# Kernel tuning notes

Measured on AMD Instinct MI355X. Metric: run time of the kernel, lower is better.

## Reference

```python
import jax, jax.numpy as jnp
import numpy as np

IGST = 10      # ghost-cell width (module-level constant in the source)
EPS = 0.01     # tol passed to NeuralODE -> runge_kutta eps
W_SCALE = 0.05 # keep the learned stencil contractive over 100 steps


def cal_boundry(u):
    # Replace the IGST ghost cells on each side with the nearest interior value.
    m, n, l = u.shape
    left = jnp.broadcast_to(u[:, :, IGST:IGST + 1], (m, n, IGST))
    right = jnp.broadcast_to(u[:, :, -IGST - 1:-IGST], (m, n, IGST))
    return jnp.concatenate([left, u[:, :, IGST:-IGST], right], axis=2)


def stencil_f(z, W):
    # func: learned 1D stencil = same-padded conv over the spatial axis.
    # z: [m, n, l], W: [n_out, n_in, k]
    return jax.lax.conv_general_dilated(
        z, W, window_strides=(1,), padding='SAME',
        dimension_numbers=('NCH', 'OIH', 'NCH'))


def setup_inputs() -> dict:
    key = jax.random.key(0)
    k1, k2 = jax.random.split(key)
    z0 = jax.random.normal(k1, (32, 16, 8192), dtype=jnp.float32)
    W = jax.random.normal(k2, (16, 16, 5), dtype=jnp.float32) * W_SCALE
    return {'z0': z0, 'W': W, 't1_t0': 1}


def reference(z0, W, t1_t0):
    # SSP-RK3 (Shu-Osher) explicit time stepping with ghost-cell BCs.
    n_steps = int(round(t1_t0 / EPS))
    h = t1_t0 / n_steps

    def step(z, _):
        k1 = cal_boundry(z + h * stencil_f(z, W))
        k2 = cal_boundry(0.75 * z + 0.25 * k1 + 0.25 * h * stencil_f(k1, W))
        z_new = cal_boundry(z / 3.0 + 2.0 * k2 / 3.0 + 2.0 * h * stencil_f(k2, W) / 3.0)
        return z_new, None

    z, _ = jax.lax.scan(step, z0, None, length=n_steps)
    return z
```

## Files before the change

kernel.cpp:

```cpp
#include <hip/hip_runtime.h>


#define NCH    16
#define LL     8192
#define TX     128
#define HALOC  32
#define SLABC  192
#define NBX    64
#define NB     32
#define NSTEPS 100
#define SPK    5
#define NKER   (NSTEPS / SPK)

#define RAD    30
#define NCHUNK 31
#define ISLAB  190

typedef __bf16 bf16x8 __attribute__((ext_vector_type(8)));
typedef __bf16 bf16x4 __attribute__((ext_vector_type(4)));
typedef float  f32x4  __attribute__((ext_vector_type(4)));

__device__ __align__(16) float g_G [ 5*256];
__device__ __align__(16) float g_G2[ 9*256];
__device__ __align__(16) float g_Tp[13*256];
__device__ __align__(16) float g_T2[25*256];
__device__ __align__(16) float g_T3[37*256];
__device__ __align__(16) float g_T4[49*256];
__device__ __align__(16) float g_T5[61*256];
__device__ __align__(16) __bf16 g_Sfrag[NCHUNK*64*8];

__global__ void build_G(const float* __restrict__ W, const int* __restrict__ tptr) {
  const float h = (float)(*tptr) / (float)NSTEPS;
  const int o = threadIdx.x >> 4, i = threadIdx.x & 15;
#pragma unroll
  for (int k = 0; k < 5; ++k)
    g_G[k*256 + o*16 + i] = h * W[o*80 + i*5 + k];
}

__global__ void compose_k(int mode) {
  const float* A; int ra; const float* B; int rb; float* C;
  switch (mode) {
    case 0:  A = g_G;  ra = 2;  B = g_G;  rb = 2; C = g_G2; break;
    case 1:  A = g_G2; ra = 4;  B = g_G;  rb = 2; C = g_Tp; break;
    case 2:  A = g_Tp; ra = 6;  B = g_Tp; rb = 6; C = g_T2; break;
    case 3:  A = g_T2; ra = 12; B = g_Tp; rb = 6; C = g_T3; break;
    case 4:  A = g_T3; ra = 18; B = g_Tp; rb = 6; C = g_T4; break;
    default: A = g_T4; ra = 24; B = g_Tp; rb = 6; C = g_T5; break;
  }
  const int rc = ra + rb;
  const int d = (int)blockIdx.x - rc;
  const int o = threadIdx.x >> 4, i = threadIdx.x & 15;
  float acc = 0.f;
  for (int a = -ra; a <= ra; ++a) {
    const int b = d - a;
    if (b < -rb || b > rb) continue;
    const float* Am = A + (a+ra)*256 + o*16;
    const float* Bm = B + (b+rb)*256 + i;
#pragma unroll
    for (int j = 0; j < 16; ++j) acc += Am[j] * Bm[j*16];
  }
  C[(size_t)blockIdx.x*256 + o*16 + i] = acc;
}

__global__ void build_Tp() {
  const int o = threadIdx.x >> 4, i = threadIdx.x & 15;
#pragma unroll
  for (int k = 0; k < 13; ++k) {
    const int d = k - 6;
    float v = g_Tp[k*256 + o*16 + i] * (1.f/6.f);
    if (d >= -4 && d <= 4) v += 0.5f * g_G2[(d+4)*256 + o*16 + i];
    if (d >= -2 && d <= 2) v += g_G[(d+2)*256 + o*16 + i];
    g_Tp[k*256 + o*16 + i] = v;
  }
}

__device__ __forceinline__ float padread(const float* M, int r, int d, int oi) {
  return (d >= -r && d <= r) ? M[(d+r)*256 + oi] : 0.f;
}

__global__ void pack_S() {
  const int c = blockIdx.x;
  const int lane = threadIdx.x & 63;
  const int jj = (threadIdx.x >> 6) * 2;
  const int gg = lane >> 4, n = lane & 15;
  const int k = 2*c + (gg >> 1);
  const int d = k - RAD;
#pragma unroll
  for (int u = 0; u < 2; ++u) {
    const int j = jj + u;
    const int i = (gg & 1)*8 + j;
    const int oi = n*16 + i;
    float v = 0.f;
    if (k <= 60) {
      v = 5.f  * padread(g_Tp,  6, d, oi)
        + 10.f * padread(g_T2, 12, d, oi)
        + 10.f * padread(g_T3, 18, d, oi)
        + 5.f  * padread(g_T4, 24, d, oi)
        +        padread(g_T5, 30, d, oi);
    }
    g_Sfrag[((size_t)c*64 + lane)*8 + j] = (__bf16)v;
  }
}

__device__ __forceinline__ int ldsIdx(int col, int ch) {
  return col * NCH + (ch ^ ((col & 4) << 1));
}

__global__ __launch_bounds__(256) void transpose_kernel(const float* __restrict__ in,
                                                        float* __restrict__ out) {
  const int b = blockIdx.y;
  const int x = blockIdx.x * 256 + threadIdx.x;
  const float* __restrict__ ib = in + (size_t)b * NCH * LL;
  float* __restrict__ ob = out + (size_t)b * NCH * LL;
  float v[NCH];
#pragma unroll
  for (int c = 0; c < NCH; ++c) v[c] = ib[c * LL + x];
#pragma unroll
  for (int c = 0; c < NCH; c += 4)
    *(float4*)(ob + (size_t)x * NCH + c) = make_float4(v[c], v[c+1], v[c+2], v[c+3]);
}

__device__ __forceinline__ bf16x8 mkA(const float* __restrict__ W, int c, int g, int n) {
  const int kk = c * 2 + (g >> 1);
  bf16x8 a;
#pragma unroll
  for (int j = 0; j < 8; ++j) {
    const int i = (g & 1) * 8 + j;
    a[j] = (__bf16)((kk < 5) ? W[n * (NCH * 5) + i * 5 + kk] : 0.0f);
  }
  return a;
}

__device__ __forceinline__ f32x4 ldState(const float* __restrict__ zb, int x0,
                                         int t, int n, int g) {
  int gx = x0 - HALOC + 16 * t + n;
  gx = min(max(gx, 0), LL - 1);
  return *(const f32x4*)(zb + (size_t)gx * NCH + g * 4);
}

template<int MODE, bool UPDZ>
__device__ __forceinline__ void tileStage(
    int t, f32x4& KZ, f32x4& KF, float az, float ak, float agh,
    const __bf16* __restrict__ RS, __bf16* __restrict__ WS,
    bf16x8 af0, bf16x8 af1, bf16x8 af2,
    int lane, int g, int n, bool leftE, bool rightE,
    float* __restrict__ ob, int x0, int finalKer)
{
  f32x4 acc = {0.f, 0.f, 0.f, 0.f};
#pragma unroll
  for (int c = 0; c < 3; ++c) {
    const int kk = c * 2 + (g >> 1);
    int s = 16 * t + n + kk - 2;
    s = min(max(s, 0), SLABC - 1);
    const bf16x8 bfrag = *(const bf16x8*)(&RS[ldsIdx(s, (g & 1) * 8)]);
    const bf16x8 a = (c == 0) ? af0 : (c == 1) ? af1 : af2;
    acc = __builtin_amdgcn_mfma_f32_16x16x32_bf16(a, bfrag, acc, 0, 0, 0);
  }
  f32x4 v;
#pragma unroll
  for (int r = 0; r < 4; ++r) v[r] = az * KZ[r] + ak * KF[r] + agh * acc[r];

  if (leftE && t == 2) {
#pragma unroll
    for (int r = 0; r < 4; ++r) {
      const float sv = __shfl(v[r], (lane & 48) | 10, 64);
      if (n < 10) v[r] = sv;
    }
  }
  if (rightE && t == 9) {
#pragma unroll
    for (int r = 0; r < 4; ++r) {
      const float sv = __shfl(v[r], (lane & 48) | 5, 64);
      if (n > 5) v[r] = sv;
    }
  }

  KF = v;
  if (UPDZ) KZ = v;

  if (MODE == 0) {
    bf16x4 bv = { (__bf16)v[0], (__bf16)v[1], (__bf16)v[2], (__bf16)v[3] };
    *(bf16x4*)(&WS[ldsIdx(16 * t + n, g * 4)]) = bv;
  } else {
    if (t >= 2 && t <= 9) {
      const int xg = x0 - HALOC + 16 * t + n;
      if (!finalKer) {
        *(f32x4*)(ob + (size_t)xg * NCH + g * 4) = v;
      } else {
#pragma unroll
        for (int r = 0; r < 4; ++r) ob[(size_t)(g * 4 + r) * LL + xg] = v[r];
      }
    }
  }
}

#define STAGE(az, ak, agh, UPDZ, MODE)                                          \
  do {                                                                          \
    const __bf16* RS_ = S[rb];                                                  \
    __bf16* WS_ = S[rb ^ 1];                                                    \
    tileStage<MODE, UPDZ>(wv + 0, kz0, kf0, az, ak, agh, RS_, WS_, af0, af1,    \
                          af2, lane, g, n, leftE, rightE, ob, x0, finalKer);    \
    tileStage<MODE, UPDZ>(wv + 4, kz1, kf1, az, ak, agh, RS_, WS_, af0, af1,    \
                          af2, lane, g, n, leftE, rightE, ob, x0, finalKer);    \
    tileStage<MODE, UPDZ>(wv + 8, kz2, kf2, az, ak, agh, RS_, WS_, af0, af1,    \
                          af2, lane, g, n, leftE, rightE, ob, x0, finalKer);    \
  } while (0)

__global__ __launch_bounds__(256)
void multistep_kernel(
    const float* __restrict__ zin,
    float* __restrict__ zout,
    const float* __restrict__ W,
    const int* __restrict__ tptr, int finalKer)
{
  __shared__ __align__(16) __bf16 S[2][SLABC * NCH];
  __shared__ __align__(16) __bf16 ISL[ISLAB * NCH];

  const int b = blockIdx.y, bx = blockIdx.x;
  const int x0 = bx * TX;
  const bool leftE = (bx == 0), rightE = (bx == NBX - 1);
  const int tid = threadIdx.x, lane = tid & 63, wv = tid >> 6;
  const int g = lane >> 4, n = lane & 15;

  const float* __restrict__ zb = zin + (size_t)b * NCH * LL;
  float* __restrict__ ob = zout + (size_t)b * NCH * LL;

  if (leftE || rightE) {
    const float h = (float)(*tptr) / (float)NSTEPS;
    const bf16x8 af0 = mkA(W, 0, g, n);
    const bf16x8 af1 = mkA(W, 1, g, n);
    const bf16x8 af2 = mkA(W, 2, g, n);

    for (int q = tid; q < SLABC * 4; q += 256) {
      const int s = q >> 2, cg = (q & 3) * 4;
      int gx = x0 - HALOC + s;
      gx = min(max(gx, 0), LL - 1);
      const float4 v = *(const float4*)(zb + (size_t)gx * NCH + cg);
      bf16x4 bv = { (__bf16)v.x, (__bf16)v.y, (__bf16)v.z, (__bf16)v.w };
      *(bf16x4*)(&S[0][ldsIdx(s, cg)]) = bv;
    }

    f32x4 kz0 = ldState(zb, x0, wv + 0, n, g);
    f32x4 kz1 = ldState(zb, x0, wv + 4, n, g);
    f32x4 kz2 = ldState(zb, x0, wv + 8, n, g);
    f32x4 kf0 = {0.f,0.f,0.f,0.f}, kf1 = kf0, kf2 = kf0;
    __syncthreads();

    const float c13 = 1.0f / 3.0f, c23 = 2.0f / 3.0f;
    int rb = 0;
#pragma unroll 1
    for (int sp = 0; sp < SPK; ++sp) {
      STAGE(1.0f, 0.0f, h, false, 0);
      __syncthreads(); rb ^= 1;
      STAGE(0.75f, 0.25f, 0.25f * h, false, 0);
      __syncthreads(); rb ^= 1;
      if (sp != SPK - 1) {
        STAGE(c13, c23, c23 * h, true, 0);
        __syncthreads(); rb ^= 1;
      } else {
        STAGE(c13, c23, c23 * h, true, 1);
      }
    }
  } else {
    for (int q = tid; q < ISLAB * 4; q += 256) {
      const int s = q >> 2, cg = (q & 3) * 4;
      const int gx = x0 - RAD + s;
      const float4 v = *(const float4*)(zb + (size_t)gx * NCH + cg);
      bf16x4 bv = { (__bf16)v.x, (__bf16)v.y, (__bf16)v.z, (__bf16)v.w };
      *(bf16x4*)(&ISL[ldsIdx(s, cg)]) = bv;
    }

    const int o0 = 16 * wv + n;
    const f32x4 kz0 = *(const f32x4*)(zb + (size_t)(x0 + o0) * NCH + g * 4);
    const f32x4 kz1 = *(const f32x4*)(zb + (size_t)(x0 + o0 + 64) * NCH + g * 4);
    __syncthreads();

    const int p = g >> 1, hsel = g & 1;
    f32x4 acc0 = {0.f,0.f,0.f,0.f}, acc1 = acc0;
    const __bf16* Af = g_Sfrag + (size_t)lane * 8;
    int col0 = o0 + p;
#pragma unroll
    for (int c = 0; c < NCHUNK; ++c) {
      const bf16x8 a = *(const bf16x8*)(Af + (size_t)c * 512);
      const int xr = ((((col0 >> 2) & 1) ^ hsel) << 4);
      const bf16x8 b0 = *(const bf16x8*)((const char*)ISL + col0 * 32 + xr);
      const bf16x8 b1 = *(const bf16x8*)((const char*)ISL + (col0 + 64) * 32 + xr);
      acc0 = __builtin_amdgcn_mfma_f32_16x16x32_bf16(a, b0, acc0, 0, 0, 0);
      acc1 = __builtin_amdgcn_mfma_f32_16x16x32_bf16(a, b1, acc1, 0, 0, 0);
      col0 += 2;
    }

    f32x4 v0, v1;
#pragma unroll
    for (int r = 0; r < 4; ++r) { v0[r] = kz0[r] + acc0[r]; v1[r] = kz1[r] + acc1[r]; }

    if (!finalKer) {
      *(f32x4*)(ob + (size_t)(x0 + o0) * NCH + g * 4) = v0;
      *(f32x4*)(ob + (size_t)(x0 + o0 + 64) * NCH + g * 4) = v1;
    } else {
#pragma unroll
      for (int r = 0; r < 4; ++r) {
        ob[(size_t)(g * 4 + r) * LL + (x0 + o0)] = v0[r];
        ob[(size_t)(g * 4 + r) * LL + (x0 + o0 + 64)] = v1[r];
      }
    }
  }
}

extern "C" void kernel_launch(void* const* d_in, const int* in_sizes, int n_in,
                              void* d_out, int out_size, void* d_ws, size_t ws_size,
                              hipStream_t stream) {
  const float* z0 = (const float*)d_in[0];
  const float* W  = (const float*)d_in[1];
  const int*   t  = (const int*)d_in[2];

  float* Q = (float*)d_out;
  float* P = (float*)d_ws;

  build_G<<<dim3(1), dim3(256), 0, stream>>>(W, t);
  compose_k<<<dim3( 9), dim3(256), 0, stream>>>(0);
  compose_k<<<dim3(13), dim3(256), 0, stream>>>(1);
  build_Tp<<<dim3(1), dim3(256), 0, stream>>>();
  compose_k<<<dim3(25), dim3(256), 0, stream>>>(2);
  compose_k<<<dim3(37), dim3(256), 0, stream>>>(3);
  compose_k<<<dim3(49), dim3(256), 0, stream>>>(4);
  compose_k<<<dim3(61), dim3(256), 0, stream>>>(5);
  pack_S<<<dim3(NCHUNK), dim3(256), 0, stream>>>();

  dim3 block(256);
  transpose_kernel<<<dim3(32, NB), block, 0, stream>>>(z0, Q);

  dim3 mgrid(NBX, NB);
  for (int k = 1; k <= NKER; ++k) {
    if (k & 1) multistep_kernel<<<mgrid, block, 0, stream>>>(Q, P, W, t, 0);
    else       multistep_kernel<<<mgrid, block, 0, stream>>>(P, Q, W, t, k == NKER);
  }
}
```

Before: 801.2 us.

## Precompute boundary-block propagators and replace iterative edge blocks with dense matvec

```diff
diff --git a/kernel.cpp b/kernel.cpp
--- a/kernel.cpp
+++ b/kernel.cpp
@@ -4,8 +4,6 @@
 #define NCH    16
 #define LL     8192
 #define TX     128
-#define HALOC  32
-#define SLABC  192
 #define NBX    64
 #define NB     32
 #define NSTEPS 100
@@ -15,6 +13,11 @@
 #define RAD    30
 #define NCHUNK 31
 #define ISLAB  190
+
+#define WCOLS  96
+#define DWIN   1072
+#define NROWS  592
+#define EBLK   4
 
 typedef __bf16 bf16x8 __attribute__((ext_vector_type(8)));
 typedef __bf16 bf16x4 __attribute__((ext_vector_type(4)));
@@ -28,6 +31,8 @@
 __device__ __align__(16) float g_T4[49*256];
 __device__ __align__(16) float g_T5[61*256];
 __device__ __align__(16) __bf16 g_Sfrag[NCHUNK*64*8];
+__device__ __align__(16) float g_CL[(size_t)NROWS*DWIN];
+__device__ __align__(16) float g_CR[(size_t)NROWS*DWIN];
 
 __global__ void build_G(const float* __restrict__ W, const int* __restrict__ tptr) {
   const float h = (float)(*tptr) / (float)NSTEPS;
@@ -106,6 +111,108 @@
   return col * NCH + (ch ^ ((col & 4) << 1));
 }
 
+__device__ __forceinline__ bf16x8 mkA(const float* __restrict__ W, int c, int g, int n) {
+  const int kk = c * 2 + (g >> 1);
+  bf16x8 a;
+#pragma unroll
+  for (int j = 0; j < 8; ++j) {
+    const int i = (g & 1) * 8 + j;
+    a[j] = (__bf16)((kk < 5) ? W[n * (NCH * 5) + i * 5 + kk] : 0.0f);
+  }
+  return a;
+}
+
+__global__ __launch_bounds__(384)
+void edge_evolve(const float* __restrict__ W, const int* __restrict__ tptr) {
+  __shared__ __align__(16) __bf16 ES[2][WCOLS * NCH];
+  const int j = blockIdx.x, e = blockIdx.y;
+  const float h = (float)(*tptr) / (float)NSTEPS;
+  const int tid = threadIdx.x, lane = tid & 63, wv = tid >> 6;
+  const int g = lane >> 4, n = lane & 15;
+  const int t = wv, mycol = 16 * t + n;
+  const int cwj = (e ? 29 : 0) + (j >> 4), chj = j & 15;
+
+  const bf16x8 af0 = mkA(W, 0, g, n);
+  const bf16x8 af1 = mkA(W, 1, g, n);
+  const bf16x8 af2 = mkA(W, 2, g, n);
+
+  const int hot = ldsIdx(cwj, chj);
+  for (int q = tid; q < WCOLS * NCH; q += 384)
+    ES[0][q] = (__bf16)(q == hot ? 1.f : 0.f);
+
+  f32x4 kz = {0.f, 0.f, 0.f, 0.f};
+  if (mycol == cwj && g == (chj >> 2)) kz[chj & 3] = 1.f;
+  f32x4 kf = {0.f, 0.f, 0.f, 0.f};
+  __syncthreads();
+
+  const float c13 = 1.0f / 3.0f, c23 = 2.0f / 3.0f;
+  int rb = 0;
+#pragma unroll 1
+  for (int sp = 0; sp < SPK; ++sp) {
+#pragma unroll 1
+    for (int st = 0; st < 3; ++st) {
+      const float az  = (st == 0) ? 1.0f : (st == 1) ? 0.75f : c13;
+      const float ak  = (st == 0) ? 0.0f : (st == 1) ? 0.25f : c23;
+      const float agh = (st == 0) ? h    : (st == 1) ? 0.25f*h : c23*h;
+      const __bf16* RS = ES[rb];
+      __bf16* WS = ES[rb ^ 1];
+      f32x4 acc = {0.f, 0.f, 0.f, 0.f};
+#pragma unroll
+      for (int c = 0; c < 3; ++c) {
+        const int kk = c * 2 + (g >> 1);
+        int s = mycol + kk - 2;
+        s = min(max(s, 0), WCOLS - 1);
+        const bf16x8 bfrag = *(const bf16x8*)(&RS[ldsIdx(s, (g & 1) * 8)]);
+        const bf16x8 a = (c == 0) ? af0 : (c == 1) ? af1 : af2;
+        acc = __builtin_amdgcn_mfma_f32_16x16x32_bf16(a, bfrag, acc, 0, 0, 0);
+      }
+      f32x4 v;
+#pragma unroll
+      for (int r = 0; r < 4; ++r) v[r] = az * kz[r] + ak * kf[r] + agh * acc[r];
+      if (e == 0 && t == 0) {
+#pragma unroll
+        for (int r = 0; r < 4; ++r) {
+          const float sv = __shfl(v[r], (lane & 48) | 10, 64);
+          if (n < 10) v[r] = sv;
+        }
+      }
+      if (e == 1 && t == 5) {
+#pragma unroll
+        for (int r = 0; r < 4; ++r) {
+          const float sv = __shfl(v[r], (lane & 48) | 5, 64);
+          if (n > 5) v[r] = sv;
+        }
+      }
+      kf = v;
+      if (st == 2) kz = v;
+      bf16x4 bv = { (__bf16)v[0], (__bf16)v[1], (__bf16)v[2], (__bf16)v[3] };
+      *(bf16x4*)(&WS[ldsIdx(mycol, g * 4)]) = bv;
+      __syncthreads();
+      rb ^= 1;
+    }
+  }
+
+  if (e == 0) {
+    if (mycol <= 36) {
+      const int rowb = mycol * 16 + g * 4;
+#pragma unroll
+      for (int r = 0; r < 4; ++r) {
+        const float id = (mycol == cwj && (g * 4 + r) == chj) ? 1.f : 0.f;
+        g_CL[(size_t)(rowb + r) * DWIN + j] = kz[r] - id;
+      }
+    }
+  } else {
+    if (mycol >= 59) {
+      const int rowb = (mycol - 59) * 16 + g * 4;
+#pragma unroll
+      for (int r = 0; r < 4; ++r) {
+        const float id = (mycol == cwj && (g * 4 + r) == chj) ? 1.f : 0.f;
+        g_CR[(size_t)(rowb + r) * DWIN + j] = kz[r] - id;
+      }
+    }
+  }
+}
+
 __global__ __launch_bounds__(256) void transpose_kernel(const float* __restrict__ in,
                                                         float* __restrict__ out) {
   const int b = blockIdx.y;
@@ -120,151 +227,30 @@
     *(float4*)(ob + (size_t)x * NCH + c) = make_float4(v[c], v[c+1], v[c+2], v[c+3]);
 }
 
-__device__ __forceinline__ bf16x8 mkA(const float* __restrict__ W, int c, int g, int n) {
-  const int kk = c * 2 + (g >> 1);
-  bf16x8 a;
-#pragma unroll
-  for (int j = 0; j < 8; ++j) {
-    const int i = (g & 1) * 8 + j;
-    a[j] = (__bf16)((kk < 5) ? W[n * (NCH * 5) + i * 5 + kk] : 0.0f);
-  }
-  return a;
-}
-
-__device__ __forceinline__ f32x4 ldState(const float* __restrict__ zb, int x0,
-                                         int t, int n, int g) {
-  int gx = x0 - HALOC + 16 * t + n;
-  gx = min(max(gx, 0), LL - 1);
-  return *(const f32x4*)(zb + (size_t)gx * NCH + g * 4);
-}
-
-template<int MODE, bool UPDZ>
-__device__ __forceinline__ void tileStage(
-    int t, f32x4& KZ, f32x4& KF, float az, float ak, float agh,
-    const __bf16* __restrict__ RS, __bf16* __restrict__ WS,
-    bf16x8 af0, bf16x8 af1, bf16x8 af2,
-    int lane, int g, int n, bool leftE, bool rightE,
-    float* __restrict__ ob, int x0, int finalKer)
-{
-  f32x4 acc = {0.f, 0.f, 0.f, 0.f};
-#pragma unroll
-  for (int c = 0; c < 3; ++c) {
-    const int kk = c * 2 + (g >> 1);
-    int s = 16 * t + n + kk - 2;
-    s = min(max(s, 0), SLABC - 1);
-    const bf16x8 bfrag = *(const bf16x8*)(&RS[ldsIdx(s, (g & 1) * 8)]);
-    const bf16x8 a = (c == 0) ? af0 : (c == 1) ? af1 : af2;
-    acc = __builtin_amdgcn_mfma_f32_16x16x32_bf16(a, bfrag, acc, 0, 0, 0);
-  }
-  f32x4 v;
-#pragma unroll
-  for (int r = 0; r < 4; ++r) v[r] = az * KZ[r] + ak * KF[r] + agh * acc[r];
-
-  if (leftE && t == 2) {
-#pragma unroll
-    for (int r = 0; r < 4; ++r) {
-      const float sv = __shfl(v[r], (lane & 48) | 10, 64);
-      if (n < 10) v[r] = sv;
-    }
-  }
-  if (rightE && t == 9) {
-#pragma unroll
-    for (int r = 0; r < 4; ++r) {
-      const float sv = __shfl(v[r], (lane & 48) | 5, 64);
-      if (n > 5) v[r] = sv;
-    }
-  }
-
-  KF = v;
-  if (UPDZ) KZ = v;
-
-  if (MODE == 0) {
-    bf16x4 bv = { (__bf16)v[0], (__bf16)v[1], (__bf16)v[2], (__bf16)v[3] };
-    *(bf16x4*)(&WS[ldsIdx(16 * t + n, g * 4)]) = bv;
-  } else {
-    if (t >= 2 && t <= 9) {
-      const int xg = x0 - HALOC + 16 * t + n;
-      if (!finalKer) {
-        *(f32x4*)(ob + (size_t)xg * NCH + g * 4) = v;
-      } else {
-#pragma unroll
-        for (int r = 0; r < 4; ++r) ob[(size_t)(g * 4 + r) * LL + xg] = v[r];
-      }
-    }
-  }
-}
-
-#define STAGE(az, ak, agh, UPDZ, MODE)                                          \
-  do {                                                                          \
-    const __bf16* RS_ = S[rb];                                                  \
-    __bf16* WS_ = S[rb ^ 1];                                                    \
-    tileStage<MODE, UPDZ>(wv + 0, kz0, kf0, az, ak, agh, RS_, WS_, af0, af1,    \
-                          af2, lane, g, n, leftE, rightE, ob, x0, finalKer);    \
-    tileStage<MODE, UPDZ>(wv + 4, kz1, kf1, az, ak, agh, RS_, WS_, af0, af1,    \
-                          af2, lane, g, n, leftE, rightE, ob, x0, finalKer);    \
-    tileStage<MODE, UPDZ>(wv + 8, kz2, kf2, az, ak, agh, RS_, WS_, af0, af1,    \
-                          af2, lane, g, n, leftE, rightE, ob, x0, finalKer);    \
-  } while (0)
-
 __global__ __launch_bounds__(256)
 void multistep_kernel(
     const float* __restrict__ zin,
     float* __restrict__ zout,
-    const float* __restrict__ W,
     const int* __restrict__ tptr, int finalKer)
 {
-  __shared__ __align__(16) __bf16 S[2][SLABC * NCH];
   __shared__ __align__(16) __bf16 ISL[ISLAB * NCH];
+  __shared__ __align__(16) float  XW[DWIN];
 
   const int b = blockIdx.y, bx = blockIdx.x;
-  const int x0 = bx * TX;
-  const bool leftE = (bx == 0), rightE = (bx == NBX - 1);
   const int tid = threadIdx.x, lane = tid & 63, wv = tid >> 6;
   const int g = lane >> 4, n = lane & 15;
 
   const float* __restrict__ zb = zin + (size_t)b * NCH * LL;
   float* __restrict__ ob = zout + (size_t)b * NCH * LL;
 
-  if (leftE || rightE) {
-    const float h = (float)(*tptr) / (float)NSTEPS;
-    const bf16x8 af0 = mkA(W, 0, g, n);
-    const bf16x8 af1 = mkA(W, 1, g, n);
-    const bf16x8 af2 = mkA(W, 2, g, n);
-
-    for (int q = tid; q < SLABC * 4; q += 256) {
-      const int s = q >> 2, cg = (q & 3) * 4;
-      int gx = x0 - HALOC + s;
-      gx = min(max(gx, 0), LL - 1);
-      const float4 v = *(const float4*)(zb + (size_t)gx * NCH + cg);
-      bf16x4 bv = { (__bf16)v.x, (__bf16)v.y, (__bf16)v.z, (__bf16)v.w };
-      *(bf16x4*)(&S[0][ldsIdx(s, cg)]) = bv;
-    }
-
-    f32x4 kz0 = ldState(zb, x0, wv + 0, n, g);
-    f32x4 kz1 = ldState(zb, x0, wv + 4, n, g);
-    f32x4 kz2 = ldState(zb, x0, wv + 8, n, g);
-    f32x4 kf0 = {0.f,0.f,0.f,0.f}, kf1 = kf0, kf2 = kf0;
-    __syncthreads();
-
-    const float c13 = 1.0f / 3.0f, c23 = 2.0f / 3.0f;
-    int rb = 0;
-#pragma unroll 1
-    for (int sp = 0; sp < SPK; ++sp) {
-      STAGE(1.0f, 0.0f, h, false, 0);
-      __syncthreads(); rb ^= 1;
-      STAGE(0.75f, 0.25f, 0.25f * h, false, 0);
-      __syncthreads(); rb ^= 1;
-      if (sp != SPK - 1) {
-        STAGE(c13, c23, c23 * h, true, 0);
-        __syncthreads(); rb ^= 1;
-      } else {
-        STAGE(c13, c23, c23 * h, true, 1);
-      }
-    }
-  } else {
+  if (bx < NBX) {
+    const int x0 = bx * TX;
+    const bool leftE = (bx == 0), rightE = (bx == NBX - 1);
+
     for (int q = tid; q < ISLAB * 4; q += 256) {
       const int s = q >> 2, cg = (q & 3) * 4;
-      const int gx = x0 - RAD + s;
+      int gx = x0 - RAD + s;
+      gx = min(max(gx, 0), LL - 1);
       const float4 v = *(const float4*)(zb + (size_t)gx * NCH + cg);
       bf16x4 bv = { (__bf16)v.x, (__bf16)v.y, (__bf16)v.z, (__bf16)v.w };
       *(bf16x4*)(&ISL[ldsIdx(s, cg)]) = bv;
@@ -294,14 +280,44 @@
 #pragma unroll
     for (int r = 0; r < 4; ++r) { v0[r] = kz0[r] + acc0[r]; v1[r] = kz1[r] + acc1[r]; }
 
+    const bool st0 = !(leftE && o0 <= 36);
+    const bool st1 = !(rightE && o0 >= 27);
     if (!finalKer) {
-      *(f32x4*)(ob + (size_t)(x0 + o0) * NCH + g * 4) = v0;
-      *(f32x4*)(ob + (size_t)(x0 + o0 + 64) * NCH + g * 4) = v1;
+      if (st0) *(f32x4*)(ob + (size_t)(x0 + o0) * NCH + g * 4) = v0;
+      if (st1) *(f32x4*)(ob + (size_t)(x0 + o0 + 64) * NCH + g * 4) = v1;
     } else {
 #pragma unroll
       for (int r = 0; r < 4; ++r) {
-        ob[(size_t)(g * 4 + r) * LL + (x0 + o0)] = v0[r];
-        ob[(size_t)(g * 4 + r) * LL + (x0 + o0 + 64)] = v1[r];
+        if (st0) ob[(size_t)(g * 4 + r) * LL + (x0 + o0)] = v0[r];
+        if (st1) ob[(size_t)(g * 4 + r) * LL + (x0 + o0 + 64)] = v1[r];
+      }
+    }
+  } else {
+    const int q = bx - NBX;
+    const int e = q >> 1, half = q & 1;
+    const float* __restrict__ xs = zb + (e ? (size_t)(LL - 67) * NCH : 0);
+    for (int i = tid; i < DWIN; i += 256) XW[i] = xs[i];
+    __syncthreads();
+
+    const int rbase = half * (NROWS / 2);
+    const float* __restrict__ C = (e ? g_CR : g_CL) + (size_t)rbase * DWIN;
+    for (int r = tid; r < NROWS / 2; r += 256) {
+      const float* __restrict__ Crow = C + (size_t)r * DWIN;
+      float acc = 0.f;
+#pragma unroll 4
+      for (int jj = 0; jj < DWIN; jj += 4) {
+        const f32x4 cf = *(const f32x4*)(Crow + jj);
+        const f32x4 xv = *(const f32x4*)(&XW[jj]);
+        acc += cf[0]*xv[0] + cf[1]*xv[1] + cf[2]*xv[2] + cf[3]*xv[3];
+      }
+      const int row = rbase + r;
+      const float out = XW[(e ? 480 : 0) + row] + acc;
+      if (e == 0) {
+        if (!finalKer) ob[row] = out;
+        else ob[(size_t)(row & 15) * LL + (row >> 4)] = out;
+      } else {
+        if (!finalKer) ob[(size_t)(LL - 37) * NCH + row] = out;
+        else ob[(size_t)(row & 15) * LL + (LL - 37 + (row >> 4))] = out;
       }
     }
   }
@@ -327,12 +343,14 @@
   compose_k<<<dim3(61), dim3(256), 0, stream>>>(5);
   pack_S<<<dim3(NCHUNK), dim3(256), 0, stream>>>();
 
+  edge_evolve<<<dim3(DWIN, 2), dim3(384), 0, stream>>>(W, t);
+
   dim3 block(256);
   transpose_kernel<<<dim3(32, NB), block, 0, stream>>>(z0, Q);
 
-  dim3 mgrid(NBX, NB);
+  dim3 mgrid(NBX + EBLK, NB);
   for (int k = 1; k <= NKER; ++k) {
-    if (k & 1) multistep_kernel<<<mgrid, block, 0, stream>>>(Q, P, W, t, 0);
-    else       multistep_kernel<<<mgrid, block, 0, stream>>>(P, Q, W, t, k == NKER);
-  }
-}
+    if (k & 1) multistep_kernel<<<mgrid, block, 0, stream>>>(Q, P, t, 0);
+    else       multistep_kernel<<<mgrid, block, 0, stream>>>(P, Q, t, k == NKER);
+  }
+}
```

New measurement: 1.654 ms. +106.4%, slower.
